# Performance work log

Hardware: AMD Instinct MI355X
Metric: run time of the kernel (lower is better)

Reference implementation:

```python
import jax, jax.numpy as jnp
import numpy as np
import math
from itertools import combinations

SEQ_LEN = 8
SET_SIZE = 3
IN_DIM = 2048
OUT_DIM = 1152
WAY = 5
SHOT = 5
N_QUERIES = 200
PE_SCALE = 0.1
LN_EPS = 1e-5
NEG_INF = -1e30

TUPLES = np.array(list(combinations(range(SEQ_LEN), SET_SIZE)), dtype=np.int32)  # [56, 3]
TUPLES_LEN = TUPLES.shape[0]


def _positional_encoding(d_model, max_len):
    position = np.arange(max_len)[:, None].astype(np.float32)
    div_term = np.exp(np.arange(0, d_model, 2).astype(np.float32) * -(math.log(10000.0) / d_model))
    pe = np.zeros((max_len, d_model), dtype=np.float32)
    pe[:, 0::2] = np.sin(position * div_term) * PE_SCALE
    pe[:, 1::2] = np.cos(position * div_term) * PE_SCALE
    return jnp.asarray(pe)

PE = _positional_encoding(IN_DIM, int(SEQ_LEN * 1.5))


def setup_inputs() -> dict:
    key = jax.random.key(0)
    ks = jax.random.split(key, 6)
    support_set = jax.random.normal(ks[0], (WAY * SHOT, SEQ_LEN, IN_DIM), dtype=jnp.float32)
    queries = jax.random.normal(ks[1], (N_QUERIES, SEQ_LEN, IN_DIM), dtype=jnp.float32)
    support_labels = jnp.repeat(jnp.arange(WAY, dtype=jnp.int32), SHOT)  # [25]
    Wk = jax.random.normal(ks[2], (IN_DIM * SET_SIZE, OUT_DIM), dtype=jnp.float32) * 0.02
    bk = jnp.zeros((OUT_DIM,), dtype=jnp.float32)
    Wv = jax.random.normal(ks[3], (IN_DIM * SET_SIZE, OUT_DIM), dtype=jnp.float32) * 0.02
    bv = jnp.zeros((OUT_DIM,), dtype=jnp.float32)
    ln_g = jnp.ones((OUT_DIM,), dtype=jnp.float32)
    ln_b = jnp.zeros((OUT_DIM,), dtype=jnp.float32)
    return {"support_set": support_set, "support_labels": support_labels, "queries": queries,
            "Wk": Wk, "bk": bk, "Wv": Wv, "bv": bv, "ln_g": ln_g, "ln_b": ln_b}


def _layernorm(x, g, b):
    mu = jnp.mean(x, axis=-1, keepdims=True)
    var = jnp.var(x, axis=-1, keepdims=True)
    return (x - mu) * jax.lax.rsqrt(var + LN_EPS) * g + b


def _tuple_features(x):
    # x: [N, SEQ_LEN, IN_DIM]; add PE (dropout is identity at inference), gather frame tuples.
    n = x.shape[0]
    x = x + PE[None, :x.shape[1], :]
    return x[:, TUPLES, :].reshape(n, TUPLES_LEN, SET_SIZE * IN_DIM)  # [N, 56, 6144]


def reference(support_set, support_labels, queries, Wk, bk, Wv, bv, ln_g, ln_b):
    n_q = queries.shape[0]
    s_feat = _tuple_features(support_set)   # [S, T, 6144]
    q_feat = _tuple_features(queries)       # [Q, T, 6144]

    sk = _layernorm(s_feat @ Wk + bk, ln_g, ln_b)  # [S, T, D]
    qk = _layernorm(q_feat @ Wk + bk, ln_g, ln_b)  # [Q, T, D]
    sv = s_feat @ Wv + bv                           # [S, T, D]
    qv = q_feat @ Wv + bv                           # [Q, T, D]

    # scores between every query tuple and every support tuple
    scores = jnp.einsum('qtd,skd->qtsk', qk, sk) / math.sqrt(OUT_DIM)  # [Q, T, S, T]

    # per-class masked softmax over (support clips of class c) x (support tuples)
    class_mask = support_labels[None, :] == jnp.arange(WAY, dtype=support_labels.dtype)[:, None]  # [WAY, S]
    masked = scores[None] + jnp.where(class_mask[:, None, None, :, None], 0.0, NEG_INF)  # [WAY, Q, T, S, T]
    attn = jax.nn.softmax(masked.reshape(WAY, n_q, TUPLES_LEN, -1), axis=-1)
    attn = attn.reshape(WAY, n_q, TUPLES_LEN, -1, TUPLES_LEN)  # [WAY, Q, T, S, T]

    proto = jnp.einsum('cqtsk,skd->cqtd', attn, sv)  # [WAY, Q, T, D]
    diff = qv[None] - proto                           # [WAY, Q, T, D]
    dist = -jnp.sum(diff * diff, axis=(2, 3)) / TUPLES_LEN  # [WAY, Q]
    return dist.T  # logits [Q, WAY]
```

## Files before the change

kernel.cpp:

```cpp
#include <hip/hip_runtime.h>
#include <math.h>

#define SEQ_LEN 8
#define IN_DIM 2048
#define OUT_DIM 1152
#define NTUP 56
#define NSUP 25
#define NQ 200
#define WAY 5
#define SFRAMES 200
#define NFRAMES 1800
#define SROWS 1400
#define QROWS 11200
#define AT_STRIDE 1440
#define KC 288
#define ALD 296

typedef __attribute__((ext_vector_type(8))) short short8;
typedef __attribute__((ext_vector_type(4))) float f32x4;

__device__ __constant__ int TUP[NTUP][3] = {
{0,1,2},{0,1,3},{0,1,4},{0,1,5},{0,1,6},{0,1,7},
{0,2,3},{0,2,4},{0,2,5},{0,2,6},{0,2,7},
{0,3,4},{0,3,5},{0,3,6},{0,3,7},
{0,4,5},{0,4,6},{0,4,7},
{0,5,6},{0,5,7},
{0,6,7},
{1,2,3},{1,2,4},{1,2,5},{1,2,6},{1,2,7},
{1,3,4},{1,3,5},{1,3,6},{1,3,7},
{1,4,5},{1,4,6},{1,4,7},
{1,5,6},{1,5,7},
{1,6,7},
{2,3,4},{2,3,5},{2,3,6},{2,3,7},
{2,4,5},{2,4,6},{2,4,7},
{2,5,6},{2,5,7},
{2,6,7},
{3,4,5},{3,4,6},{3,4,7},
{3,5,6},{3,5,7},
{3,6,7},
{4,5,6},{4,5,7},
{4,6,7},
{5,6,7}};

__device__ __forceinline__ unsigned short f2bf(float x) {
  union { float f; unsigned int u; } v; v.f = x;
  unsigned int r = v.u + 0x7fffu + ((v.u >> 16) & 1u);
  return (unsigned short)(r >> 16);
}
__device__ __forceinline__ float bf2f(unsigned short s) {
  union { float f; unsigned int u; } v; v.u = ((unsigned int)s) << 16;
  return v.f;
}

__device__ __forceinline__ void gll16(const void* g, void* l) {
  __builtin_amdgcn_global_load_lds(
      (const __attribute__((address_space(1))) unsigned int*)g,
      (__attribute__((address_space(3))) unsigned int*)l, 16, 0, 0);
}

#define APB_OFF   0UL
#define WT_OFF    7372800UL
#define PB_OFF    35684352UL
#define QKB_OFF   60567552UL
#define SKB_OFF   86372352UL
#define QVB_OFF   89597952UL
#define SVB_OFF   115402752UL
#define G2_OFF    118628352UL
#define SCB_OFF   119457792UL
#define G1B_OFF   151713792UL
#define QNORM_OFF 183969792UL
#define RANK_OFF  184014592UL

__global__ __launch_bounds__(256) void k_pre(const float* __restrict__ S,
                                             const float* __restrict__ Q,
                                             const float* __restrict__ Wk,
                                             const float* __restrict__ Wv,
                                             const int* __restrict__ labels,
                                             unsigned short* __restrict__ APb,
                                             unsigned short* __restrict__ WT,
                                             int* __restrict__ rank,
                                             float* __restrict__ outz) {
  __shared__ float t[32][33];
  int b = blockIdx.x, tid = threadIdx.x;
  if (b < NFRAMES) {
    int frame = b;
    int e8 = tid * 8;
    int pos = frame & 7;
    const float c0 = -logf(10000.0f) / (float)IN_DIM;
    float pe[8];
#pragma unroll
    for (int p = 0; p < 4; ++p) {
      float dt = expf((float)(e8 + 2 * p) * c0);
      float arg = (float)pos * dt;
      pe[2 * p] = sinf(arg) * 0.1f;
      pe[2 * p + 1] = cosf(arg) * 0.1f;
    }
    const float* src = (frame < SFRAMES) ? (S + (size_t)frame * IN_DIM + e8)
                                         : (Q + (size_t)(frame - SFRAMES) * IN_DIM + e8);
    float4 x0 = ((const float4*)src)[0], x1 = ((const float4*)src)[1];
    short8 o;
    o[0] = (short)f2bf(x0.x + pe[0]); o[1] = (short)f2bf(x0.y + pe[1]);
    o[2] = (short)f2bf(x0.z + pe[2]); o[3] = (short)f2bf(x0.w + pe[3]);
    o[4] = (short)f2bf(x1.x + pe[4]); o[5] = (short)f2bf(x1.y + pe[5]);
    o[6] = (short)f2bf(x1.z + pe[6]); o[7] = (short)f2bf(x1.w + pe[7]);
    *(short8*)(APb + (size_t)frame * IN_DIM + e8) = o;
  } else if (b < NFRAMES + 13824) {
    int z = b - NFRAMES;
    int bz = z / (64 * 36); int rem = z % (64 * 36);
    int by = rem / 64, bx = rem % 64;
    int w = bz / 3, j = bz % 3;
    const float* W = w ? Wv : Wk;
    int k0 = bx * 32, d0 = by * 32;
    int tx = tid & 31, ty = tid >> 5;
#pragma unroll
    for (int i = 0; i < 4; ++i) {
      int k = k0 + ty + i * 8;
      t[ty + i * 8][tx] = W[(size_t)(j * IN_DIM + k) * OUT_DIM + d0 + tx];
    }
    __syncthreads();
    int colbase = w * 3456 + j * 1152 + d0;
#pragma unroll
    for (int i = 0; i < 4; ++i) {
      int d = ty + i * 8;
      WT[(size_t)(colbase + d) * IN_DIM + k0 + tx] = f2bf(t[tx][d]);
    }
  } else {
    for (int i = tid; i < NQ * WAY; i += 256) outz[i] = 0.f;
    if (tid == 0) {
      for (int s = 0; s < NSUP; ++s) {
        int r = 0;
        for (int s2 = 0; s2 < NSUP; ++s2)
          r += (labels[s2] < labels[s]) || (labels[s2] == labels[s] && s2 < s);
        rank[s] = r;
      }
    }
  }
}

__device__ __forceinline__ void mfma_core(const short* __restrict__ A, int lda, int maxA,
                                          const short* __restrict__ B, int ldb, int maxB,
                                          int K, short* lds, f32x4 (&acc)[4][4]) {
  int tid = threadIdx.x;
  int lane = tid & 63, wave = tid >> 6;
  int wm = wave & 1, wn = wave >> 1;
  int col = lane & 15, quad = lane >> 4;
  short* As = lds;
  short* Bs = lds + 4096;
  int s0 = tid, s1 = tid + 256;
  int r0 = s0 >> 2, r1 = s1 >> 2;
  int o0 = (s0 & 3) * 8, o1 = (s1 & 3) * 8;
  const short* a0p = A + (size_t)min(r0, maxA) * lda + o0;
  const short* a1p = A + (size_t)min(r1, maxA) * lda + o1;
  const short* b0p = B + (size_t)min(r0, maxB) * ldb + o0;
  const short* b1p = B + (size_t)min(r1, maxB) * ldb + o1;
  short* la0 = As + s0 * 8; short* la1 = As + s1 * 8;
  short* lb0 = Bs + s0 * 8; short* lb1 = Bs + s1 * 8;

  for (int k0 = 0; k0 < K; k0 += 32) {
    gll16(a0p + k0, la0);
    gll16(a1p + k0, la1);
    gll16(b0p + k0, lb0);
    gll16(b1p + k0, lb1);
    __syncthreads();
    short8 af[4], bf[4];
#pragma unroll
    for (int i = 0; i < 4; ++i)
      af[i] = *(const short8*)(As + (wm * 64 + i * 16 + col) * 32 + quad * 8);
#pragma unroll
    for (int j = 0; j < 4; ++j)
      bf[j] = *(const short8*)(Bs + (wn * 64 + j * 16 + col) * 32 + quad * 8);
#pragma unroll
    for (int i = 0; i < 4; ++i)
#pragma unroll
      for (int j = 0; j < 4; ++j)
        acc[i][j] = __builtin_amdgcn_mfma_f32_16x16x32_bf16(af[i], bf[j], acc[i][j], 0, 0, 0);
    __syncthreads();
  }
}

__global__ __launch_bounds__(256) void k_gemm1(const unsigned short* __restrict__ APb,
                                               const unsigned short* __restrict__ WT,
                                               unsigned short* __restrict__ Pb) {
  __shared__ short lds[8192];
  int row0 = blockIdx.y * 128, col0 = blockIdx.x * 128;
  f32x4 acc[4][4];
#pragma unroll
  for (int i = 0; i < 4; ++i)
#pragma unroll
    for (int j = 0; j < 4; ++j) acc[i][j] = (f32x4)(0.f);
  mfma_core((const short*)APb + (size_t)row0 * IN_DIM, IN_DIM, min(127, NFRAMES - 1 - row0),
            (const short*)WT + (size_t)col0 * IN_DIM, IN_DIM, 127,
            IN_DIM, lds, acc);
  int lane = threadIdx.x & 63, wave = threadIdx.x >> 6;
  int wm = wave & 1, wn = wave >> 1, col = lane & 15, quad = lane >> 4;
#pragma unroll
  for (int i = 0; i < 4; ++i)
#pragma unroll
    for (int r = 0; r < 4; ++r) {
      int gr = row0 + wm * 64 + i * 16 + quad * 4 + r;
      if (gr >= NFRAMES) continue;
#pragma unroll
      for (int j = 0; j < 4; ++j)
        Pb[(size_t)gr * 6912 + col0 + wn * 64 + j * 16 + col] = f2bf(acc[i][j][r]);
    }
}

__global__ __launch_bounds__(256) void k_combine(const unsigned short* __restrict__ Pb,
                                                 const float* __restrict__ bk,
                                                 const float* __restrict__ bv,
                                                 const float* __restrict__ g,
                                                 const float* __restrict__ bb,
                                                 const int* __restrict__ rank,
                                                 unsigned short* __restrict__ SKb,
                                                 unsigned short* __restrict__ QKb,
                                                 unsigned short* __restrict__ SVb,
                                                 unsigned short* __restrict__ QVb,
                                                 float* __restrict__ qnorm) {
  __shared__ short L[8 * 3456];
  int n = blockIdx.x, w = blockIdx.y;
  int tid = threadIdx.x;
  bool sup = n < NSUP;
  int fbase = sup ? n * SEQ_LEN : SFRAMES + (n - NSUP) * SEQ_LEN;
  for (int i = 0; i < 14; ++i) {
    int idx = tid + 256 * i;
    if (idx < 3456) {
      int fr = idx / 432, off = (idx - fr * 432) * 8;
      *(short8*)(L + fr * 3456 + off) =
          *(const short8*)(Pb + (size_t)(fbase + fr) * 6912 + w * 3456 + off);
    }
  }
  __syncthreads();
  int wave = tid >> 6, lane = tid & 63;
  const float* bias = w ? bv : bk;
  float2 bi[9], gg[9], bbv[9];
#pragma unroll
  for (int i = 0; i < 9; ++i) {
    int p = lane + 64 * i;
    bi[i] = *(const float2*)(bias + 2 * p);
    if (w == 0) {
      gg[i] = *(const float2*)(g + 2 * p);
      bbv[i] = *(const float2*)(bb + 2 * p);
    }
  }
  int obase = sup ? rank[n] * NTUP : (n - NSUP) * NTUP;
  const unsigned int* Lu = (const unsigned int*)L;
  for (int t = wave; t < NTUP; t += 4) {
    int b0 = (TUP[t][0] * 3456) >> 1;
    int b1 = (TUP[t][1] * 3456 + 1152) >> 1;
    int b2 = (TUP[t][2] * 3456 + 2304) >> 1;
    float va[18];
    float sum = 0.f, sq = 0.f;
#pragma unroll
    for (int i = 0; i < 9; ++i) {
      int p = lane + 64 * i;
      unsigned int u0 = Lu[b0 + p], u1 = Lu[b1 + p], u2 = Lu[b2 + p];
      float a = bf2f((unsigned short)u0) + bf2f((unsigned short)u1) +
                bf2f((unsigned short)u2) + bi[i].x;
      float b = bf2f((unsigned short)(u0 >> 16)) + bf2f((unsigned short)(u1 >> 16)) +
                bf2f((unsigned short)(u2 >> 16)) + bi[i].y;
      va[2 * i] = a; va[2 * i + 1] = b;
      sum += a + b;
      sq += a * a + b * b;
    }
#pragma unroll
    for (int o = 32; o; o >>= 1) {
      sum += __shfl_xor(sum, o);
      sq += __shfl_xor(sq, o);
    }
    int orow = obase + t;
    if (w == 0) {
      float mean = sum * (1.f / OUT_DIM);
      float var = sq * (1.f / OUT_DIM) - mean * mean;
      float inv = rsqrtf(var + 1e-5f);
      unsigned short* outp = (sup ? SKb : QKb) + (size_t)orow * OUT_DIM;
#pragma unroll
      for (int i = 0; i < 9; ++i) {
        int p = lane + 64 * i;
        unsigned int lo = f2bf((va[2 * i] - mean) * inv * gg[i].x + bbv[i].x);
        unsigned int hi = f2bf((va[2 * i + 1] - mean) * inv * gg[i].y + bbv[i].y);
        *(unsigned int*)(outp + 2 * p) = lo | (hi << 16);
      }
    } else {
      unsigned short* outp = (sup ? SVb : QVb) + (size_t)orow * OUT_DIM;
#pragma unroll
      for (int i = 0; i < 9; ++i) {
        int p = lane + 64 * i;
        unsigned int lo = f2bf(va[2 * i]);
        unsigned int hi = f2bf(va[2 * i + 1]);
        *(unsigned int*)(outp + 2 * p) = lo | (hi << 16);
      }
      if (!sup && lane == 0) qnorm[orow] = sq;
    }
  }
}

__global__ __launch_bounds__(256) void k_rowgemm(const unsigned short* __restrict__ QKb,
                                                 const unsigned short* __restrict__ SKb,
                                                 const unsigned short* __restrict__ QVb,
                                                 const unsigned short* __restrict__ SVb,
                                                 unsigned short* __restrict__ SCb,
                                                 unsigned short* __restrict__ G1b,
                                                 unsigned short* __restrict__ G2) {
  __shared__ short lds[8192];
  int L = blockIdx.x;
  f32x4 acc[4][4];
#pragma unroll
  for (int i = 0; i < 4; ++i)
#pragma unroll
    for (int j = 0; j < 4; ++j) acc[i][j] = (f32x4)(0.f);
  int lane = threadIdx.x & 63, wave = threadIdx.x >> 6;
  int wm = wave & 1, wn = wave >> 1, col = lane & 15, quad = lane >> 4;

  if (L < 1936) {
    int l = L, g1 = 0;
    if (l >= 968) { g1 = 1; l -= 968; }
    int rowSub = l & 7, t = l >> 3;
    int colIdx = t % 11, rowGroup = t / 11;
    int row0 = (rowGroup * 8 + rowSub) << 7;
    int col0 = colIdx << 7;
    const unsigned short* Am = g1 ? QVb : QKb;
    const unsigned short* Bm = g1 ? SVb : SKb;
    mfma_core((const short*)Am + (size_t)row0 * OUT_DIM, OUT_DIM, min(127, QROWS - 1 - row0),
              (const short*)Bm + (size_t)col0 * OUT_DIM, OUT_DIM, min(127, SROWS - 1 - col0),
              OUT_DIM, lds, acc);
    unsigned short* outp = g1 ? G1b : SCb;
    const float scl = g1 ? 1.0f : 0.029462782549439483f;
#pragma unroll
    for (int i = 0; i < 4; ++i)
#pragma unroll
      for (int r = 0; r < 4; ++r) {
        int gr = row0 + wm * 64 + i * 16 + quad * 4 + r;
        if (gr >= QROWS) continue;
#pragma unroll
        for (int j = 0; j < 4; ++j) {
          int gc = col0 + wn * 64 + j * 16 + col;
          if (gc < SROWS) {
            int c = gc / 280;
            outp[(size_t)gr * AT_STRIDE + gc + c * 8] = f2bf(acc[i][j][r] * scl);
          }
        }
      }
  } else {
    int l = L - 1936;
    int c = l / 9, rem = l % 9;
    int i0 = (rem / 3) << 7, j0 = (rem % 3) << 7;
    const short* base = (const short*)SVb + (size_t)c * 280 * OUT_DIM;
    mfma_core(base + (size_t)i0 * OUT_DIM, OUT_DIM, min(127, 279 - i0),
              base + (size_t)j0 * OUT_DIM, OUT_DIM, min(127, 279 - j0),
              OUT_DIM, lds, acc);
    unsigned short* g2c = G2 + (size_t)c * KC * KC;
#pragma unroll
    for (int i = 0; i < 4; ++i)
#pragma unroll
      for (int r = 0; r < 4; ++r) {
        int gi = i0 + wm * 64 + i * 16 + quad * 4 + r;
        if (gi >= KC) continue;
#pragma unroll
        for (int j = 0; j < 4; ++j) {
          int gj = j0 + wn * 64 + j * 16 + col;
          if (gj < KC) g2c[(size_t)gi * KC + gj] = f2bf(acc[i][j][r]);
        }
      }
  }
}

__global__ __launch_bounds__(256) void k_attn(const unsigned short* __restrict__ SCb,
                                              const unsigned short* __restrict__ G1b,
                                              const unsigned short* __restrict__ G2,
                                              const float* __restrict__ qnorm,
                                              float* __restrict__ out) {
  __shared__ short attn[64 * ALD];
  __shared__ short Bs[4096];
  __shared__ float rowsum[64];
  __shared__ float T2n[64];
  __shared__ float Sarr[64];
  __shared__ float val[64];
  int r0 = blockIdx.x * 64, c = blockIdx.y;
  int tid = threadIdx.x;
  int lane = tid & 63, wave = tid >> 6;
  int col = lane & 15, quad = lane >> 4;

  int lr = tid >> 2, h = tid & 3;
  const unsigned short* ps = SCb + (size_t)(r0 + lr) * AT_STRIDE + c * KC;
  const unsigned short* pg = G1b + (size_t)(r0 + lr) * AT_STRIDE + c * KC;
  short8 sv[9];
  float mx = -INFINITY;
#pragma unroll
  for (int i = 0; i < 9; ++i) {
    int v = h * 9 + i;
    if (v < 35) {
      sv[i] = *(const short8*)(ps + v * 8);
#pragma unroll
      for (int j = 0; j < 8; ++j) mx = fmaxf(mx, bf2f((unsigned short)sv[i][j]));
    }
  }
  mx = fmaxf(mx, __shfl_xor(mx, 1));
  mx = fmaxf(mx, __shfl_xor(mx, 2));
  float sum = 0.f, t2 = 0.f;
#pragma unroll
  for (int i = 0; i < 9; ++i) {
    int v = h * 9 + i;
    if (v < 35) {
      short8 gv8 = *(const short8*)(pg + v * 8);
      short8 e8;
#pragma unroll
      for (int j = 0; j < 8; ++j) {
        float e = __expf(bf2f((unsigned short)sv[i][j]) - mx);
        sum += e;
        t2 += e * bf2f((unsigned short)gv8[j]);
        e8[j] = (short)f2bf(e);
      }
      *(short8*)(attn + lr * ALD + v * 8) = e8;
    } else {
      *(short8*)(attn + lr * ALD + v * 8) = (short8)0;
    }
  }
  sum += __shfl_xor(sum, 1); sum += __shfl_xor(sum, 2);
  t2 += __shfl_xor(t2, 1); t2 += __shfl_xor(t2, 2);
  if (h == 0) { Sarr[lr] = sum; T2n[lr] = t2; }
  if (tid < 64) rowsum[tid] = 0.f;
  __syncthreads();

  const unsigned short* G2c = G2 + (size_t)c * KC * KC;
  float part[4][4] = {};
  for (int j0 = 0; j0 < KC; j0 += 128) {
    int maxB = KC - 1 - j0;
    f32x4 acc[4][2];
#pragma unroll
    for (int i = 0; i < 4; ++i) { acc[i][0] = (f32x4)(0.f); acc[i][1] = (f32x4)(0.f); }
    bool active = (wave * 32) <= maxB;
    for (int k0 = 0; k0 < KC; k0 += 32) {
      int s = tid, row = s >> 2, off = (s & 3) * 8;
      gll16(G2c + (size_t)(j0 + min(row, maxB)) * KC + k0 + off, Bs + s * 8);
      s = tid + 256; row = s >> 2; off = (s & 3) * 8;
      gll16(G2c + (size_t)(j0 + min(row, maxB)) * KC + k0 + off, Bs + s * 8);
      __syncthreads();
      if (active) {
        short8 af[4], bf[2];
#pragma unroll
        for (int i = 0; i < 4; ++i)
          af[i] = *(const short8*)(attn + (i * 16 + col) * ALD + k0 + quad * 8);
#pragma unroll
        for (int j = 0; j < 2; ++j)
          bf[j] = *(const short8*)(Bs + (wave * 32 + j * 16 + col) * 32 + quad * 8);
#pragma unroll
        for (int i = 0; i < 4; ++i)
#pragma unroll
          for (int j = 0; j < 2; ++j)
            acc[i][j] = __builtin_amdgcn_mfma_f32_16x16x32_bf16(af[i], bf[j], acc[i][j], 0, 0, 0);
      }
      __syncthreads();
    }
    if (active) {
#pragma unroll
      for (int i = 0; i < 4; ++i)
#pragma unroll
        for (int r = 0; r < 4; ++r) {
          int rl = i * 16 + quad * 4 + r;
#pragma unroll
          for (int j = 0; j < 2; ++j) {
            int gj = j0 + wave * 32 + j * 16 + col;
            if (gj < KC)
              part[i][r] += bf2f((unsigned short)attn[rl * ALD + gj]) * acc[i][j][r];
          }
        }
    }
  }
#pragma unroll
  for (int i = 0; i < 4; ++i)
#pragma unroll
    for (int r = 0; r < 4; ++r) {
      float s = part[i][r];
      s += __shfl_xor(s, 1); s += __shfl_xor(s, 2);
      s += __shfl_xor(s, 4); s += __shfl_xor(s, 8);
      if (col == 0) atomicAdd(&rowsum[i * 16 + quad * 4 + r], s);
    }
  __syncthreads();

  if (tid < 64) {
    float S = Sarr[tid];
    float invS = 1.f / S;
    val[tid] = qnorm[r0 + tid] - 2.f * T2n[tid] * invS + rowsum[tid] * invS * invS;
  }
  __syncthreads();
  if (tid < 3) {
    int q = r0 / NTUP + tid;
    int lo = max(q * NTUP, r0), hi = min(q * NTUP + NTUP, r0 + 64);
    if (lo < hi && q < NQ) {
      float s = 0.f;
      for (int r = lo; r < hi; ++r) s += val[r - r0];
      atomicAdd(&out[q * WAY + c], -s * (1.f / NTUP));
    }
  }
}

extern "C" void kernel_launch(void* const* d_in, const int* in_sizes, int n_in,
                              void* d_out, int out_size, void* d_ws, size_t ws_size,
                              hipStream_t stream) {
  const float* support = (const float*)d_in[0];
  const int* labels = (const int*)d_in[1];
  const float* queries = (const float*)d_in[2];
  const float* Wk = (const float*)d_in[3];
  const float* bk = (const float*)d_in[4];
  const float* Wv = (const float*)d_in[5];
  const float* bv = (const float*)d_in[6];
  const float* ln_g = (const float*)d_in[7];
  const float* ln_b = (const float*)d_in[8];
  float* out = (float*)d_out;
  char* w8 = (char*)d_ws;

  unsigned short* APb = (unsigned short*)(w8 + APB_OFF);
  unsigned short* WT = (unsigned short*)(w8 + WT_OFF);
  unsigned short* Pb = (unsigned short*)(w8 + PB_OFF);
  unsigned short* QKb = (unsigned short*)(w8 + QKB_OFF);
  unsigned short* SKb = (unsigned short*)(w8 + SKB_OFF);
  unsigned short* QVb = (unsigned short*)(w8 + QVB_OFF);
  unsigned short* SVb = (unsigned short*)(w8 + SVB_OFF);
  unsigned short* G2 = (unsigned short*)(w8 + G2_OFF);
  unsigned short* SCb = (unsigned short*)(w8 + SCB_OFF);
  unsigned short* G1b = (unsigned short*)(w8 + G1B_OFF);
  float* QNORM = (float*)(w8 + QNORM_OFF);
  int* RANK = (int*)(w8 + RANK_OFF);

  k_pre<<<dim3(NFRAMES + 13824 + 1), dim3(256), 0, stream>>>(support, queries, Wk, Wv,
                                                             labels, APb, WT, RANK, out);
  k_gemm1<<<dim3(54, 15), dim3(256), 0, stream>>>(APb, WT, Pb);
  k_combine<<<dim3(225, 2), dim3(256), 0, stream>>>(Pb, bk, bv, ln_g, ln_b, RANK,
                                                    SKb, QKb, SVb, QVb, QNORM);
  k_rowgemm<<<dim3(1981), dim3(256), 0, stream>>>(QKb, SKb, QVb, SVb, SCb, G1b, G2);
  k_attn<<<dim3(175, 5), dim3(256), 0, stream>>>(SCb, G1b, G2, QNORM, out);
}
```

Before: 399.1 us.

## Split attention into softmax kernel and tiled attn·G2·attn quadratic-form GEMM kernel

The fused attention kernel is split in two. A softmax kernel writes unnormalised bf16 attention weights plus per-row base and inverse-sum terms to global memory. A second kernel computes the quadratic form attn·G2·attnᵀ using the shared 128x128 mfma_core tile, with all four waves active across the full tile. This is meant to remove the poor MFMA utilisation of the old 64-row tile, where some waves sat idle on the last column block. In exchange it adds an extra launch and a global round-trip of the attention matrix, and the epilogue re-reads attention values from global memory.

Result: slower. 439.4 us (+10.1%).

```diff
diff --git a/kernel.cpp b/kernel.cpp
--- a/kernel.cpp
+++ b/kernel.cpp
@@ -14,7 +14,6 @@
 #define QROWS 11200
 #define AT_STRIDE 1440
 #define KC 288
-#define ALD 296
 
 typedef __attribute__((ext_vector_type(8))) short short8;
 typedef __attribute__((ext_vector_type(4))) float f32x4;
@@ -68,8 +67,11 @@
 #define G2_OFF    118628352UL
 #define SCB_OFF   119457792UL
 #define G1B_OFF   151713792UL
-#define QNORM_OFF 183969792UL
-#define RANK_OFF  184014592UL
+#define ATB_OFF   183969792UL
+#define QNORM_OFF 216225792UL
+#define BASE_OFF  216270592UL
+#define INV_OFF   216494592UL
+#define RANK_OFF  216718592UL
 
 __global__ __launch_bounds__(256) void k_pre(const float* __restrict__ S,
                                              const float* __restrict__ Q,
@@ -364,25 +366,19 @@
   }
 }
 
-__global__ __launch_bounds__(256) void k_attn(const unsigned short* __restrict__ SCb,
-                                              const unsigned short* __restrict__ G1b,
-                                              const unsigned short* __restrict__ G2,
-                                              const float* __restrict__ qnorm,
-                                              float* __restrict__ out) {
-  __shared__ short attn[64 * ALD];
-  __shared__ short Bs[4096];
-  __shared__ float rowsum[64];
-  __shared__ float T2n[64];
-  __shared__ float Sarr[64];
-  __shared__ float val[64];
+__global__ __launch_bounds__(256) void k_softmax(const unsigned short* __restrict__ SCb,
+                                                 const unsigned short* __restrict__ G1b,
+                                                 const float* __restrict__ qnorm,
+                                                 unsigned short* __restrict__ ATb,
+                                                 float* __restrict__ BASE,
+                                                 float* __restrict__ INV) {
   int r0 = blockIdx.x * 64, c = blockIdx.y;
   int tid = threadIdx.x;
-  int lane = tid & 63, wave = tid >> 6;
-  int col = lane & 15, quad = lane >> 4;
-
   int lr = tid >> 2, h = tid & 3;
-  const unsigned short* ps = SCb + (size_t)(r0 + lr) * AT_STRIDE + c * KC;
-  const unsigned short* pg = G1b + (size_t)(r0 + lr) * AT_STRIDE + c * KC;
+  int row = r0 + lr;
+  const unsigned short* ps = SCb + (size_t)row * AT_STRIDE + c * KC;
+  const unsigned short* pg = G1b + (size_t)row * AT_STRIDE + c * KC;
+  unsigned short* pa = ATb + (size_t)row * AT_STRIDE + c * KC;
   short8 sv[9];
   float mx = -INFINITY;
 #pragma unroll
@@ -410,61 +406,62 @@
         t2 += e * bf2f((unsigned short)gv8[j]);
         e8[j] = (short)f2bf(e);
       }
-      *(short8*)(attn + lr * ALD + v * 8) = e8;
+      *(short8*)(pa + v * 8) = e8;
     } else {
-      *(short8*)(attn + lr * ALD + v * 8) = (short8)0;
+      *(short8*)(pa + v * 8) = (short8)0;
     }
   }
   sum += __shfl_xor(sum, 1); sum += __shfl_xor(sum, 2);
   t2 += __shfl_xor(t2, 1); t2 += __shfl_xor(t2, 2);
-  if (h == 0) { Sarr[lr] = sum; T2n[lr] = t2; }
-  if (tid < 64) rowsum[tid] = 0.f;
-  __syncthreads();
-
-  const unsigned short* G2c = G2 + (size_t)c * KC * KC;
+  if (h == 0) {
+    float invS = 1.f / sum;
+    BASE[(size_t)c * QROWS + row] = qnorm[row] - 2.f * t2 * invS;
+    INV[(size_t)c * QROWS + row] = invS * invS;
+  }
+}
+
+__global__ __launch_bounds__(256) void k_b2t3(const unsigned short* __restrict__ ATb,
+                                              const unsigned short* __restrict__ G2,
+                                              const float* __restrict__ BASE,
+                                              const float* __restrict__ INV,
+                                              float* __restrict__ out) {
+  __shared__ short lds[8192];
+  __shared__ float rowsum[128];
+  __shared__ float val[128];
+  int r0 = blockIdx.x * 128, c = blockIdx.y;
+  int tid = threadIdx.x;
+  if (tid < 128) rowsum[tid] = 0.f;
+  int lane = tid & 63, wave = tid >> 6;
+  int wm = wave & 1, wn = wave >> 1, quad = lane >> 4, col = lane & 15;
+  const short* A = (const short*)ATb + (size_t)r0 * AT_STRIDE + c * KC;
+  int maxA = min(127, QROWS - 1 - r0);
+  const short* G2c = (const short*)G2 + (size_t)c * KC * KC;
   float part[4][4] = {};
-  for (int j0 = 0; j0 < KC; j0 += 128) {
-    int maxB = KC - 1 - j0;
-    f32x4 acc[4][2];
-#pragma unroll
-    for (int i = 0; i < 4; ++i) { acc[i][0] = (f32x4)(0.f); acc[i][1] = (f32x4)(0.f); }
-    bool active = (wave * 32) <= maxB;
-    for (int k0 = 0; k0 < KC; k0 += 32) {
-      int s = tid, row = s >> 2, off = (s & 3) * 8;
-      gll16(G2c + (size_t)(j0 + min(row, maxB)) * KC + k0 + off, Bs + s * 8);
-      s = tid + 256; row = s >> 2; off = (s & 3) * 8;
-      gll16(G2c + (size_t)(j0 + min(row, maxB)) * KC + k0 + off, Bs + s * 8);
-      __syncthreads();
-      if (active) {
-        short8 af[4], bf[2];
-#pragma unroll
-        for (int i = 0; i < 4; ++i)
-          af[i] = *(const short8*)(attn + (i * 16 + col) * ALD + k0 + quad * 8);
-#pragma unroll
-        for (int j = 0; j < 2; ++j)
-          bf[j] = *(const short8*)(Bs + (wave * 32 + j * 16 + col) * 32 + quad * 8);
-#pragma unroll
-        for (int i = 0; i < 4; ++i)
-#pragma unroll
-          for (int j = 0; j < 2; ++j)
-            acc[i][j] = __builtin_amdgcn_mfma_f32_16x16x32_bf16(af[i], bf[j], acc[i][j], 0, 0, 0);
-      }
-      __syncthreads();
-    }
-    if (active) {
-#pragma unroll
-      for (int i = 0; i < 4; ++i)
-#pragma unroll
-        for (int r = 0; r < 4; ++r) {
-          int rl = i * 16 + quad * 4 + r;
-#pragma unroll
-          for (int j = 0; j < 2; ++j) {
-            int gj = j0 + wave * 32 + j * 16 + col;
-            if (gj < KC)
-              part[i][r] += bf2f((unsigned short)attn[rl * ALD + gj]) * acc[i][j][r];
+#pragma unroll
+  for (int jt = 0; jt < 3; ++jt) {
+    int j0 = jt * 128;
+    f32x4 acc[4][4];
+#pragma unroll
+    for (int i = 0; i < 4; ++i)
+#pragma unroll
+      for (int j = 0; j < 4; ++j) acc[i][j] = (f32x4)(0.f);
+    mfma_core(A, AT_STRIDE, maxA,
+              G2c + (size_t)j0 * KC, KC, min(127, KC - 1 - j0),
+              KC, lds, acc);
+#pragma unroll
+    for (int i = 0; i < 4; ++i)
+#pragma unroll
+      for (int r = 0; r < 4; ++r) {
+        int gr = r0 + wm * 64 + i * 16 + quad * 4 + r;
+        if (gr < QROWS) {
+          const unsigned short* ar = ATb + (size_t)gr * AT_STRIDE + c * KC;
+#pragma unroll
+          for (int j = 0; j < 4; ++j) {
+            int gj = j0 + wn * 64 + j * 16 + col;
+            if (gj < KC) part[i][r] += bf2f(ar[gj]) * acc[i][j][r];
           }
         }
-    }
+      }
   }
 #pragma unroll
   for (int i = 0; i < 4; ++i)
@@ -473,23 +470,25 @@
       float s = part[i][r];
       s += __shfl_xor(s, 1); s += __shfl_xor(s, 2);
       s += __shfl_xor(s, 4); s += __shfl_xor(s, 8);
-      if (col == 0) atomicAdd(&rowsum[i * 16 + quad * 4 + r], s);
+      if (col == 0) atomicAdd(&rowsum[wm * 64 + i * 16 + quad * 4 + r], s);
     }
   __syncthreads();
-
-  if (tid < 64) {
-    float S = Sarr[tid];
-    float invS = 1.f / S;
-    val[tid] = qnorm[r0 + tid] - 2.f * T2n[tid] * invS + rowsum[tid] * invS * invS;
+  if (tid < 128) {
+    int gr = r0 + tid;
+    val[tid] = (gr < QROWS)
+                   ? BASE[(size_t)c * QROWS + gr] + rowsum[tid] * INV[(size_t)c * QROWS + gr]
+                   : 0.f;
   }
   __syncthreads();
-  if (tid < 3) {
+  if (tid < 4) {
     int q = r0 / NTUP + tid;
-    int lo = max(q * NTUP, r0), hi = min(q * NTUP + NTUP, r0 + 64);
-    if (lo < hi && q < NQ) {
-      float s = 0.f;
-      for (int r = lo; r < hi; ++r) s += val[r - r0];
-      atomicAdd(&out[q * WAY + c], -s * (1.f / NTUP));
+    if (q < NQ) {
+      int lo = max(q * NTUP, r0), hi = min(q * NTUP + NTUP, min(r0 + 128, QROWS));
+      if (lo < hi) {
+        float s = 0.f;
+        for (int r = lo; r < hi; ++r) s += val[r - r0];
+        atomicAdd(&out[q * WAY + c], -s * (1.f / NTUP));
+      }
     }
   }
 }
@@ -519,7 +518,10 @@
   unsigned short* G2 = (unsigned short*)(w8 + G2_OFF);
   unsigned short* SCb = (unsigned short*)(w8 + SCB_OFF);
   unsigned short* G1b = (unsigned short*)(w8 + G1B_OFF);
+  unsigned short* ATb = (unsigned short*)(w8 + ATB_OFF);
   float* QNORM = (float*)(w8 + QNORM_OFF);
+  float* BASE = (float*)(w8 + BASE_OFF);
+  float* INV = (float*)(w8 + INV_OFF);
   int* RANK = (int*)(w8 + RANK_OFF);
 
   k_pre<<<dim3(NFRAMES + 13824 + 1), dim3(256), 0, stream>>>(support, queries, Wk, Wv,
@@ -528,5 +530,6 @@
   k_combine<<<dim3(225, 2), dim3(256), 0, stream>>>(Pb, bk, bv, ln_g, ln_b, RANK,
                                                     SKb, QKb, SVb, QVb, QNORM);
   k_rowgemm<<<dim3(1981), dim3(256), 0, stream>>>(QKb, SKb, QVb, SVb, SCb, G1b, G2);
-  k_attn<<<dim3(175, 5), dim3(256), 0, stream>>>(SCb, G1b, G2, QNORM, out);
-}
+  k_softmax<<<dim3(175, 5), dim3(256), 0, stream>>>(SCb, G1b, QNORM, ATb, BASE, INV);
+  k_b2t3<<<dim3(88, 5), dim3(256), 0, stream>>>(ATb, G2, BASE, INV, out);
+}
```

## Repartition attention quadratic form per wave over rows, read G2 directly from global

Applied to the files above, without the earlier changes.

Restructures the quadratic-form step in k_attn so that each wave owns 16 attention rows and all 288 output columns (18 accumulator tiles). The G2 operand is now read straight from global/L2 instead of being staged through shared memory. This removes the shared-memory B staging, the many __syncthreads per k-step, the idle waves on the partial last column chunk, and the shared rowsum atomics. In exchange it uses more accumulator registers and issues redundant global loads of G2 across waves, which may lower occupancy or become bound on L2 bandwidth.

Result: slower. 455.6 us (+14.2%).

```diff
diff --git a/kernel.cpp b/kernel.cpp
--- a/kernel.cpp
+++ b/kernel.cpp
@@ -370,15 +370,11 @@
                                               const float* __restrict__ qnorm,
                                               float* __restrict__ out) {
   __shared__ short attn[64 * ALD];
-  __shared__ short Bs[4096];
-  __shared__ float rowsum[64];
   __shared__ float T2n[64];
   __shared__ float Sarr[64];
   __shared__ float val[64];
   int r0 = blockIdx.x * 64, c = blockIdx.y;
   int tid = threadIdx.x;
-  int lane = tid & 63, wave = tid >> 6;
-  int col = lane & 15, quad = lane >> 4;
 
   int lr = tid >> 2, h = tid & 3;
   const unsigned short* ps = SCb + (size_t)(r0 + lr) * AT_STRIDE + c * KC;
@@ -418,71 +414,41 @@
   sum += __shfl_xor(sum, 1); sum += __shfl_xor(sum, 2);
   t2 += __shfl_xor(t2, 1); t2 += __shfl_xor(t2, 2);
   if (h == 0) { Sarr[lr] = sum; T2n[lr] = t2; }
-  if (tid < 64) rowsum[tid] = 0.f;
   __syncthreads();
 
-  const unsigned short* G2c = G2 + (size_t)c * KC * KC;
-  float part[4][4] = {};
-  for (int j0 = 0; j0 < KC; j0 += 128) {
-    int maxB = KC - 1 - j0;
-    f32x4 acc[4][2];
-#pragma unroll
-    for (int i = 0; i < 4; ++i) { acc[i][0] = (f32x4)(0.f); acc[i][1] = (f32x4)(0.f); }
-    bool active = (wave * 32) <= maxB;
-    for (int k0 = 0; k0 < KC; k0 += 32) {
-      int s = tid, row = s >> 2, off = (s & 3) * 8;
-      gll16(G2c + (size_t)(j0 + min(row, maxB)) * KC + k0 + off, Bs + s * 8);
-      s = tid + 256; row = s >> 2; off = (s & 3) * 8;
-      gll16(G2c + (size_t)(j0 + min(row, maxB)) * KC + k0 + off, Bs + s * 8);
-      __syncthreads();
-      if (active) {
-        short8 af[4], bf[2];
-#pragma unroll
-        for (int i = 0; i < 4; ++i)
-          af[i] = *(const short8*)(attn + (i * 16 + col) * ALD + k0 + quad * 8);
-#pragma unroll
-        for (int j = 0; j < 2; ++j)
-          bf[j] = *(const short8*)(Bs + (wave * 32 + j * 16 + col) * 32 + quad * 8);
-#pragma unroll
-        for (int i = 0; i < 4; ++i)
-#pragma unroll
-          for (int j = 0; j < 2; ++j)
-            acc[i][j] = __builtin_amdgcn_mfma_f32_16x16x32_bf16(af[i], bf[j], acc[i][j], 0, 0, 0);
-      }
-      __syncthreads();
-    }
-    if (active) {
-#pragma unroll
-      for (int i = 0; i < 4; ++i)
-#pragma unroll
-        for (int r = 0; r < 4; ++r) {
-          int rl = i * 16 + quad * 4 + r;
-#pragma unroll
-          for (int j = 0; j < 2; ++j) {
-            int gj = j0 + wave * 32 + j * 16 + col;
-            if (gj < KC)
-              part[i][r] += bf2f((unsigned short)attn[rl * ALD + gj]) * acc[i][j][r];
-          }
-        }
-    }
-  }
-#pragma unroll
-  for (int i = 0; i < 4; ++i)
-#pragma unroll
-    for (int r = 0; r < 4; ++r) {
-      float s = part[i][r];
-      s += __shfl_xor(s, 1); s += __shfl_xor(s, 2);
-      s += __shfl_xor(s, 4); s += __shfl_xor(s, 8);
-      if (col == 0) atomicAdd(&rowsum[i * 16 + quad * 4 + r], s);
-    }
+  int lane = tid & 63, wave = tid >> 6;
+  int col = lane & 15, quad = lane >> 4;
+  const short* G2c = (const short*)G2 + (size_t)c * KC * KC;
+  const short* arow = attn + (wave * 16 + col) * ALD;
+  f32x4 acc[18];
+#pragma unroll
+  for (int j = 0; j < 18; ++j) acc[j] = (f32x4)(0.f);
+#pragma unroll
+  for (int kq = 0; kq < 9; ++kq) {
+    int k0 = kq * 32;
+    short8 af = *(const short8*)(arow + k0 + quad * 8);
+#pragma unroll
+    for (int j = 0; j < 18; ++j) {
+      short8 bf = *(const short8*)(G2c + (size_t)(j * 16 + col) * KC + k0 + quad * 8);
+      acc[j] = __builtin_amdgcn_mfma_f32_16x16x32_bf16(af, bf, acc[j], 0, 0, 0);
+    }
+  }
+#pragma unroll
+  for (int r = 0; r < 4; ++r) {
+    int m = wave * 16 + quad * 4 + r;
+    float s = 0.f;
+#pragma unroll
+    for (int j = 0; j < 18; ++j)
+      s += bf2f((unsigned short)attn[m * ALD + j * 16 + col]) * acc[j][r];
+    s += __shfl_xor(s, 1); s += __shfl_xor(s, 2);
+    s += __shfl_xor(s, 4); s += __shfl_xor(s, 8);
+    if (col == 0) {
+      float S = Sarr[m], invS = 1.f / S;
+      val[m] = qnorm[r0 + m] - 2.f * T2n[m] * invS + s * invS * invS;
+    }
+  }
   __syncthreads();
 
-  if (tid < 64) {
-    float S = Sarr[tid];
-    float invS = 1.f / S;
-    val[tid] = qnorm[r0 + tid] - 2.f * T2n[tid] * invS + rowsum[tid] * invS * invS;
-  }
-  __syncthreads();
   if (tid < 3) {
     int q = r0 / NTUP + tid;
     int lo = max(q * NTUP, r0), hi = min(q * NTUP + NTUP, r0 + 64);
```
